# Optimization experiments

Measured on AMD Instinct MI355X. Metric: run time of the kernel, lower is better.

Reference implementation:

```python
import jax, jax.numpy as jnp
import numpy as np

EMBED_DIM = 2048
NUM_HEADS = 16
HEAD_DIM = EMBED_DIM // NUM_HEADS


def setup_inputs() -> dict:
    key = jax.random.key(0)
    k_x, k_qkv, k_out = jax.random.split(key, 3)
    x = jax.random.normal(k_x, (4, 2048, EMBED_DIM), dtype=jnp.float32)
    # torch nn.Linear(in, out) weight is [out, in]; y = x @ W.T
    scale = 1.0 / np.sqrt(EMBED_DIM)
    W_qkv = jax.random.uniform(k_qkv, (3 * EMBED_DIM, EMBED_DIM), dtype=jnp.float32, minval=-scale, maxval=scale)
    W_out = jax.random.uniform(k_out, (EMBED_DIM, EMBED_DIM), dtype=jnp.float32, minval=-scale, maxval=scale)
    return {"x": x, "W_qkv": W_qkv, "W_out": W_out}


def reference(x, W_qkv, W_out):
    B, T, C = x.shape
    H, D = NUM_HEADS, HEAD_DIM
    qkv = jnp.einsum("btc,fc->btf", x, W_qkv)  # [B,T,3C]
    q, k, v = jnp.split(qkv, 3, axis=-1)
    q = q.reshape(B, T, H, D).transpose(0, 2, 1, 3)  # [B,H,T,D]
    k = k.reshape(B, T, H, D).transpose(0, 2, 1, 3)
    v = v.reshape(B, T, H, D).transpose(0, 2, 1, 3)
    att = jnp.einsum("bhqd,bhkd->bhqk", q, k) / jnp.sqrt(jnp.float32(D))
    causal = jnp.tril(jnp.ones((T, T), dtype=bool))
    att = jnp.where(causal[None, None], att, -jnp.inf)
    att = jax.nn.softmax(att, axis=-1)
    out = jnp.einsum("bhqk,bhkd->bhqd", att, v)  # [B,H,T,D]
    out = out.transpose(0, 2, 1, 3).reshape(B, T, C)
    return jnp.einsum("btc,oc->bto", out, W_out)
```

## Files before the change

### kernel.cpp

```cpp
#include <hip/hip_runtime.h>
#include <hip/hip_bf16.h>
#include <math.h>

#define BDIM 4
#define TDIM 2048
#define CDIM 2048
#define HDIM 16
#define DDIM 128
#define MROWS (BDIM*TDIM)
#define NQKV (3*CDIM)
#define GK   CDIM
#define QSZ  (MROWS*CDIM)

#define NTILES 32
#define NITER  16
#define HT     8192
#define BOFF   32768

#define QSCALE 0.1275171f

typedef __attribute__((ext_vector_type(8))) short short8;
typedef __attribute__((ext_vector_type(4))) unsigned short ushort4v;
typedef __attribute__((ext_vector_type(4))) float f32x4;

__device__ __forceinline__ unsigned short f2bf(float f) {
    unsigned int u = __float_as_uint(f);
    u += 0x7fffu + ((u >> 16) & 1u);
    return (unsigned short)(u >> 16);
}

__device__ __forceinline__ void gload16(const unsigned short* g, unsigned short* l) {
    __builtin_amdgcn_global_load_lds((__attribute__((address_space(1))) void*)(g),
                                     (__attribute__((address_space(3))) void*)(l),
                                     16, 0, 0);
}

__global__ __launch_bounds__(256) void cvt_bf16(const float* __restrict__ in,
                                                unsigned short* __restrict__ outp,
                                                int n4, int sbound)
{
    const int stride = gridDim.x * blockDim.x;
    for (int i = blockIdx.x * blockDim.x + threadIdx.x; i < n4; i += stride) {
        float4 f = ((const float4*)in)[i];
        const float s = (i < sbound) ? QSCALE : 1.0f;
        ushort4v u;
        u[0] = f2bf(f.x*s); u[1] = f2bf(f.y*s); u[2] = f2bf(f.z*s); u[3] = f2bf(f.w*s);
        ((ushort4v*)outp)[i] = u;
    }
}

__device__ __forceinline__ void stage_half(const unsigned short* __restrict__ T,
                                           int rowbase, int kcol,
                                           unsigned short* dst, int w, int lane)
{
    const int sw = ((lane & 3) ^ ((lane >> 3) & 3)) * 8;
#pragma unroll
    for (int j = 0; j < 2; ++j) {
        const int r = w*32 + j*16 + (lane >> 2);
        gload16(T + (size_t)(rowbase + r)*GK + kcol + sw, dst + (w*32 + j*16)*32);
    }
}

template<int MQ, int KS, int BUF, bool RDB, bool WAIT>
__device__ __forceinline__ void gphase(unsigned short* lds,
    const unsigned short* __restrict__ stT, int stRow, int stKcol, unsigned short* stDst,
    int wr, int wc, int fr, int colu, int w, int lane,
    short8 (&bfr)[4], f32x4 (&acc)[8][4])
{
    const unsigned short* Ah = lds + (BUF*2 + KS)*HT;
    const unsigned short* Bh = lds + BOFF + (BUF*2 + KS)*HT;
    short8 af[4];
#pragma unroll
    for (int mi = 0; mi < 4; ++mi)
        af[mi] = *(const short8*)&Ah[(wr*128 + (MQ*4 + mi)*16 + fr)*32 + colu];
    if (RDB) {
#pragma unroll
        for (int nj = 0; nj < 4; ++nj)
            bfr[nj] = *(const short8*)&Bh[(wc*64 + nj*16 + fr)*32 + colu];
    }
    stage_half(stT, stRow, stKcol, stDst, w, lane);
    if (WAIT) asm volatile("s_waitcnt vmcnt(4)" ::: "memory");
    __builtin_amdgcn_s_barrier();
    asm volatile("s_waitcnt lgkmcnt(0)" ::: "memory");
    __builtin_amdgcn_sched_barrier(0);
    __builtin_amdgcn_s_setprio(1);
#pragma unroll
    for (int mi = 0; mi < 4; ++mi)
#pragma unroll
        for (int nj = 0; nj < 4; ++nj)
            acc[MQ*4 + mi][nj] = __builtin_amdgcn_mfma_f32_16x16x32_bf16(af[mi], bfr[nj], acc[MQ*4 + mi][nj], 0, 0, 0);
    __builtin_amdgcn_s_setprio(0);
    __builtin_amdgcn_s_barrier();
}

template<int MODE>
__global__ __launch_bounds__(512, 2) void gemm8(const unsigned short* __restrict__ A,
                                                const unsigned short* __restrict__ B,
                                                float* __restrict__ outp,
                                                unsigned short* __restrict__ qb,
                                                unsigned short* __restrict__ kb,
                                                unsigned short* __restrict__ vt,
                                                int Nsz)
{
    extern __shared__ unsigned short lds[];
    const int tid  = threadIdx.x;
    const int w    = tid >> 6;
    const int lane = tid & 63;
    const int wr   = w >> 2, wc = w & 3;
    const int fr   = lane & 15;
    const int fg   = lane >> 4;
    const int colu = (fg ^ ((fr >> 1) & 3)) * 8;
    const int m0   = blockIdx.x * 256, n0 = blockIdx.y * 256;

    f32x4 acc[8][4];
#pragma unroll
    for (int i = 0; i < 8; ++i)
#pragma unroll
        for (int j = 0; j < 4; ++j) acc[i][j] = (f32x4)(0.f);
    short8 bfr[4];

    stage_half(A, m0, 0,  lds,             w, lane);
    stage_half(B, n0, 0,  lds + BOFF,      w, lane);
    stage_half(A, m0, 32, lds + HT,        w, lane);
    stage_half(B, n0, 32, lds + BOFF + HT, w, lane);
    stage_half(A, m0, 64, lds + 2*HT,        w, lane);
    stage_half(B, n0, 64, lds + BOFF + 2*HT, w, lane);
    asm volatile("s_waitcnt vmcnt(0)" ::: "memory");
    __builtin_amdgcn_s_barrier();

    for (int i = 0; i < NITER; ++i) {
        const int t1 = 2*i + 1;
        const int t2 = (2*i + 2 < NTILES) ? 2*i + 2 : 0;
        const int t3 = (2*i + 3 < NTILES) ? 2*i + 3 : 0;
        gphase<0,0,0,true ,false>(lds, A, m0, t1*64+32, lds + 3*HT,        wr, wc, fr, colu, w, lane, bfr, acc);
        gphase<1,0,0,false,false>(lds, B, n0, t1*64+32, lds + BOFF + 3*HT, wr, wc, fr, colu, w, lane, bfr, acc);
        gphase<0,1,0,true ,false>(lds, A, m0, t2*64,    lds,               wr, wc, fr, colu, w, lane, bfr, acc);
        gphase<1,1,0,false,true >(lds, B, n0, t2*64,    lds + BOFF,        wr, wc, fr, colu, w, lane, bfr, acc);
        gphase<0,0,1,true ,false>(lds, A, m0, t2*64+32, lds + HT,          wr, wc, fr, colu, w, lane, bfr, acc);
        gphase<1,0,1,false,false>(lds, B, n0, t2*64+32, lds + BOFF + HT,   wr, wc, fr, colu, w, lane, bfr, acc);
        gphase<0,1,1,true ,false>(lds, A, m0, t3*64,    lds + 2*HT,        wr, wc, fr, colu, w, lane, bfr, acc);
        gphase<1,1,1,false,true >(lds, B, n0, t3*64,    lds + BOFF + 2*HT, wr, wc, fr, colu, w, lane, bfr, acc);
    }
    asm volatile("s_waitcnt vmcnt(0)" ::: "memory");

    if (MODE == 0) {
#pragma unroll
        for (int mi = 0; mi < 8; ++mi)
#pragma unroll
            for (int nj = 0; nj < 4; ++nj) {
                const int n   = n0 + wc*64 + nj*16 + fr;
                const int sel = n >> 11;
                const int c   = n & 2047;
                const int hh  = c >> 7, dd = c & 127;
                const int mb  = m0 + wr*128 + mi*16 + fg*4;
                const int bb  = mb >> 11, tt = mb & 2047;
                if (sel == 2) {
                    ushort4v v;
#pragma unroll
                    for (int r = 0; r < 4; ++r) v[r] = f2bf(acc[mi][nj][r]);
                    *(ushort4v*)&vt[((size_t)(bb*HDIM + hh)*DDIM + dd)*TDIM + tt] = v;
                } else {
                    unsigned short* dstb = (sel == 0) ? qb : kb;
#pragma unroll
                    for (int r = 0; r < 4; ++r)
                        dstb[((size_t)(bb*HDIM + hh)*TDIM + tt + r)*DDIM + dd] = f2bf(acc[mi][nj][r]);
                }
            }
    } else {
#pragma unroll
        for (int mi = 0; mi < 8; ++mi)
#pragma unroll
            for (int nj = 0; nj < 4; ++nj) {
                const int n = n0 + wc*64 + nj*16 + fr;
#pragma unroll
                for (int r = 0; r < 4; ++r) {
                    const int m = m0 + wr*128 + mi*16 + fg*4 + r;
                    outp[(size_t)m*Nsz + n] = acc[mi][nj][r];
                }
            }
    }
}

__global__ __launch_bounds__(512) void attn_mfma(const unsigned short* __restrict__ Qg,
                                                 const unsigned short* __restrict__ Kg,
                                                 const unsigned short* __restrict__ Vt,
                                                 unsigned short* __restrict__ attb)
{
    extern __shared__ unsigned short smem[];
    unsigned short* KsB = smem;
    unsigned short* Vs  = smem + 16384;
    unsigned short* Ps  = smem + 24576;

    const int tid  = threadIdx.x;
    const int w    = tid >> 6;
    const int lane = tid & 63;
    const int g    = lane >> 4;
    const int c    = lane & 15;
    const int bh   = blockIdx.x & 63;
    const int qb_  = 15 - (blockIdx.x >> 6);
    const int q0   = qb_ * 128;
    const int qt   = 2*qb_ + 1;
    const int qw   = q0 + w*16;

    const unsigned short* Kbh  = Kg + (size_t)bh*TDIM*DDIM;
    const unsigned short* Vtbh = Vt + (size_t)bh*DDIM*TDIM;

    short8 qf[4];
    {
        const unsigned short* qrow = Qg + ((size_t)bh*TDIM + qw + c)*DDIM + g*8;
#pragma unroll
        for (int s = 0; s < 4; ++s)
            qf[s] = *(const short8*)(qrow + s*32);
    }

    f32x4 oacc[8];
#pragma unroll
    for (int i = 0; i < 8; ++i) oacc[i] = (f32x4)(0.f);
    float m_r[4], l_r[4];
#pragma unroll
    for (int r = 0; r < 4; ++r) { m_r[r] = -INFINITY; l_r[r] = 0.f; }

#define STAGE_K(buf, kt_)                                                        \
    {                                                                            \
        _Pragma("unroll")                                                        \
        for (int j = 0; j < 2; ++j) {                                            \
            const int rw  = (w<<3) + (j<<2) + (lane >> 4);                       \
            const int sub = (lane & 15) ^ (rw & 7);                              \
            gload16(Kbh + ((size_t)((kt_)*64 + rw))*DDIM + sub*8,                \
                    &KsB[(buf)*8192 + ((w<<3) + (j<<2))*128]);                   \
        }                                                                        \
    }
#define STAGE_V(kt_)                                                             \
    {                                                                            \
        _Pragma("unroll")                                                        \
        for (int j = 0; j < 2; ++j) {                                            \
            const int d   = (w<<4) + (j<<3) + (lane >> 3);                       \
            const int sub = (lane & 7) ^ (d & 7);                                \
            gload16(Vtbh + (size_t)d*TDIM + (kt_)*64 + sub*8,                    \
                    &Vs[((w<<4) + (j<<3))*64]);                                  \
        }                                                                        \
    }

    STAGE_K(0, 0);
    STAGE_V(0);
    __syncthreads();

    for (int kt = 0; kt <= qt; ++kt) {
        const int cur = kt & 1;
        if (kt < qt) STAGE_K(cur ^ 1, kt + 1);
        if (kt > 0)  STAGE_V(kt);

        const bool active = (kt*64) <= (qw + 15);
        short8 pf[2];

        if (active) {
            f32x4 sa[4];
#pragma unroll
            for (int n = 0; n < 4; ++n) sa[n] = (f32x4)(0.f);
#pragma unroll
            for (int s = 0; s < 4; ++s)
#pragma unroll
                for (int n = 0; n < 4; ++n) {
                    const int row = n*16 + c;
                    short8 bf = *(const short8*)&KsB[cur*8192 + ((row*128 + s*32 + g*8) ^ ((row&7)<<3))];
                    sa[n] = __builtin_amdgcn_mfma_f32_16x16x32_bf16(qf[s], bf, sa[n], 0, 0, 0);
                }

            if (kt*64 + 63 > qw) {
#pragma unroll
                for (int n = 0; n < 4; ++n) {
                    const int kgl = kt*64 + n*16 + c;
#pragma unroll
                    for (int r = 0; r < 4; ++r) {
                        const int qgl = qw + g*4 + r;
                        if (kgl > qgl) sa[n][r] = -INFINITY;
                    }
                }
            }

            float corr[4];
#pragma unroll
            for (int r = 0; r < 4; ++r) {
                float mx = fmaxf(fmaxf(sa[0][r], sa[1][r]), fmaxf(sa[2][r], sa[3][r]));
                mx = fmaxf(mx, __shfl_xor(mx, 1));
                mx = fmaxf(mx, __shfl_xor(mx, 2));
                mx = fmaxf(mx, __shfl_xor(mx, 4));
                mx = fmaxf(mx, __shfl_xor(mx, 8));
                const float mn = fmaxf(m_r[r], mx);
                corr[r] = exp2f(m_r[r] - mn);
                float rs = 0.f;
#pragma unroll
                for (int n = 0; n < 4; ++n) {
                    const float p = exp2f(sa[n][r] - mn);
                    sa[n][r] = p;
                    rs += p;
                }
                rs += __shfl_xor(rs, 1);
                rs += __shfl_xor(rs, 2);
                rs += __shfl_xor(rs, 4);
                rs += __shfl_xor(rs, 8);
                l_r[r] = l_r[r]*corr[r] + rs;
                m_r[r] = mn;
            }
#pragma unroll
            for (int i = 0; i < 8; ++i) {
                f32x4 o = oacc[i];
                o[0] *= corr[0]; o[1] *= corr[1]; o[2] *= corr[2]; o[3] *= corr[3];
                oacc[i] = o;
            }

            unsigned short* Pw = &Ps[w*1024];
#pragma unroll
            for (int n = 0; n < 4; ++n)
#pragma unroll
                for (int r = 0; r < 4; ++r) {
                    const int q = g*4 + r, k = n*16 + c;
                    Pw[(q*64 + k) ^ ((q&7)<<3)] = f2bf(sa[n][r]);
                }
#pragma unroll
            for (int s2 = 0; s2 < 2; ++s2)
                pf[s2] = *(const short8*)&Pw[(c*64 + s2*32 + g*8) ^ ((c&7)<<3)];
        }

        __syncthreads();

        if (active) {
#pragma unroll
            for (int s2 = 0; s2 < 2; ++s2)
#pragma unroll
                for (int dt = 0; dt < 8; ++dt) {
                    const int d = dt*16 + c;
                    short8 vf = *(const short8*)&Vs[(d*64 + s2*32 + g*8) ^ ((d&7)<<3)];
                    oacc[dt] = __builtin_amdgcn_mfma_f32_16x16x32_bf16(pf[s2], vf, oacc[dt], 0, 0, 0);
                }
        }

        __syncthreads();
    }

    float inv[4];
#pragma unroll
    for (int r = 0; r < 4; ++r) inv[r] = 1.f / l_r[r];
    const int b = bh >> 4, h = bh & 15;
    unsigned short* obase = attb + ((size_t)b*TDIM + qw + g*4)*CDIM + h*DDIM + c;
#pragma unroll
    for (int dt = 0; dt < 8; ++dt)
#pragma unroll
        for (int r = 0; r < 4; ++r)
            obase[(size_t)r*CDIM + dt*16] = f2bf(oacc[dt][r] * inv[r]);
}

extern "C" void kernel_launch(void* const* d_in, const int* in_sizes, int n_in,
                              void* d_out, int out_size, void* d_ws, size_t ws_size,
                              hipStream_t stream)
{
    const float* x    = (const float*)d_in[0];
    const float* Wqkv = (const float*)d_in[1];
    const float* Wout = (const float*)d_in[2];
    float* out = (float*)d_out;

    unsigned short* ws = (unsigned short*)d_ws;
    unsigned short* xb    = ws;
    unsigned short* Wqkvb = xb    + (size_t)MROWS*CDIM;
    unsigned short* Woutb = Wqkvb + (size_t)NQKV*CDIM;
    unsigned short* Qb    = Woutb + (size_t)CDIM*CDIM;
    unsigned short* Kb    = Qb + QSZ;
    unsigned short* Vtb   = Kb + QSZ;
    unsigned short* attb  = Vtb + QSZ;

    cvt_bf16<<<2048, 256, 0, stream>>>(x,    xb,    MROWS*CDIM/4, 0);
    cvt_bf16<<<2048, 256, 0, stream>>>(Wqkv, Wqkvb, NQKV*CDIM/4, CDIM*CDIM/4);
    cvt_bf16<<<1024, 256, 0, stream>>>(Wout, Woutb, CDIM*CDIM/4, 0);
    gemm8<0><<<dim3(MROWS/256, NQKV/256), 512, 131072, stream>>>(xb, Wqkvb, nullptr, Qb, Kb, Vtb, NQKV);
    attn_mfma<<<dim3(64*16), 512, 65536, stream>>>(Qb, Kb, Vtb, attb);
    gemm8<1><<<dim3(MROWS/256, CDIM/256), 512, 131072, stream>>>(attb, Woutb, out, nullptr, nullptr, nullptr, CDIM);
}
```

Before: 458.8 us.

## Double-buffer V tiles, lazily rescale softmax, and compute row sums via MFMA

V tiles are now double-buffered like K, which removes one of the two block barriers per key tile and lets V loads for the next tile overlap compute. The online softmax skips the max reduction and accumulator rescale unless some probability exceeds a threshold (the lazy-rescale trick). Row sums are computed by an MFMA against a vector of ones instead of shuffle reductions. Shared memory rises from 64 KB to 80 KB per block, which may lower occupancy. The lazy rescale keeps results exact but lets intermediate values grow larger before renormalising.

```diff
diff --git a/kernel.cpp b/kernel.cpp
--- a/kernel.cpp
+++ b/kernel.cpp
@@ -188,8 +188,8 @@
 {
     extern __shared__ unsigned short smem[];
     unsigned short* KsB = smem;
-    unsigned short* Vs  = smem + 16384;
-    unsigned short* Ps  = smem + 24576;
+    unsigned short* VsB = smem + 16384;
+    unsigned short* Ps  = smem + 32768;
 
     const int tid  = threadIdx.x;
     const int w    = tid >> 6;
@@ -213,6 +213,10 @@
             qf[s] = *(const short8*)(qrow + s*32);
     }
 
+    short8 onesf;
+#pragma unroll
+    for (int j = 0; j < 8; ++j) onesf[j] = (short)0x3F80;
+
     f32x4 oacc[8];
 #pragma unroll
     for (int i = 0; i < 8; ++i) oacc[i] = (f32x4)(0.f);
@@ -230,28 +234,26 @@
                     &KsB[(buf)*8192 + ((w<<3) + (j<<2))*128]);                   \
         }                                                                        \
     }
-#define STAGE_V(kt_)                                                             \
+#define STAGE_V(buf, kt_)                                                        \
     {                                                                            \
         _Pragma("unroll")                                                        \
         for (int j = 0; j < 2; ++j) {                                            \
             const int d   = (w<<4) + (j<<3) + (lane >> 3);                       \
             const int sub = (lane & 7) ^ (d & 7);                                \
             gload16(Vtbh + (size_t)d*TDIM + (kt_)*64 + sub*8,                    \
-                    &Vs[((w<<4) + (j<<3))*64]);                                  \
+                    &VsB[(buf)*8192 + ((w<<4) + (j<<3))*64]);                    \
         }                                                                        \
     }
 
     STAGE_K(0, 0);
-    STAGE_V(0);
+    STAGE_V(0, 0);
     __syncthreads();
 
     for (int kt = 0; kt <= qt; ++kt) {
         const int cur = kt & 1;
-        if (kt < qt) STAGE_K(cur ^ 1, kt + 1);
-        if (kt > 0)  STAGE_V(kt);
+        if (kt < qt) { STAGE_K(cur ^ 1, kt + 1); STAGE_V(cur ^ 1, kt + 1); }
 
         const bool active = (kt*64) <= (qw + 15);
-        short8 pf[2];
 
         if (active) {
             f32x4 sa[4];
@@ -278,35 +280,48 @@
                 }
             }
 
-            float corr[4];
-#pragma unroll
-            for (int r = 0; r < 4; ++r) {
-                float mx = fmaxf(fmaxf(sa[0][r], sa[1][r]), fmaxf(sa[2][r], sa[3][r]));
-                mx = fmaxf(mx, __shfl_xor(mx, 1));
-                mx = fmaxf(mx, __shfl_xor(mx, 2));
-                mx = fmaxf(mx, __shfl_xor(mx, 4));
-                mx = fmaxf(mx, __shfl_xor(mx, 8));
-                const float mn = fmaxf(m_r[r], mx);
-                corr[r] = exp2f(m_r[r] - mn);
-                float rs = 0.f;
-#pragma unroll
-                for (int n = 0; n < 4; ++n) {
-                    const float p = exp2f(sa[n][r] - mn);
-                    sa[n][r] = p;
-                    rs += p;
-                }
-                rs += __shfl_xor(rs, 1);
-                rs += __shfl_xor(rs, 2);
-                rs += __shfl_xor(rs, 4);
-                rs += __shfl_xor(rs, 8);
-                l_r[r] = l_r[r]*corr[r] + rs;
-                m_r[r] = mn;
-            }
-#pragma unroll
-            for (int i = 0; i < 8; ++i) {
-                f32x4 o = oacc[i];
-                o[0] *= corr[0]; o[1] *= corr[1]; o[2] *= corr[2]; o[3] *= corr[3];
-                oacc[i] = o;
+            f32x4 p[4];
+            bool slow = (kt == 0);
+            if (!slow) {
+#pragma unroll
+                for (int n = 0; n < 4; ++n)
+#pragma unroll
+                    for (int r = 0; r < 4; ++r)
+                        p[n][r] = exp2f(sa[n][r] - m_r[r]);
+                float pm = p[0][0];
+#pragma unroll
+                for (int n = 0; n < 4; ++n)
+#pragma unroll
+                    for (int r = 0; r < 4; ++r)
+                        pm = fmaxf(pm, p[n][r]);
+                slow = __any(pm > 256.0f);
+            }
+            if (slow) {
+                float corr[4];
+#pragma unroll
+                for (int r = 0; r < 4; ++r) {
+                    float mx = fmaxf(fmaxf(sa[0][r], sa[1][r]), fmaxf(sa[2][r], sa[3][r]));
+                    mx = fmaxf(mx, __shfl_xor(mx, 1));
+                    mx = fmaxf(mx, __shfl_xor(mx, 2));
+                    mx = fmaxf(mx, __shfl_xor(mx, 4));
+                    mx = fmaxf(mx, __shfl_xor(mx, 8));
+                    const float mn = fmaxf(m_r[r], mx);
+                    corr[r] = exp2f(m_r[r] - mn);
+                    m_r[r] = mn;
+                }
+#pragma unroll
+                for (int n = 0; n < 4; ++n)
+#pragma unroll
+                    for (int r = 0; r < 4; ++r)
+                        p[n][r] = exp2f(sa[n][r] - m_r[r]);
+#pragma unroll
+                for (int i = 0; i < 8; ++i) {
+                    f32x4 o = oacc[i];
+                    o[0] *= corr[0]; o[1] *= corr[1]; o[2] *= corr[2]; o[3] *= corr[3];
+                    oacc[i] = o;
+                }
+#pragma unroll
+                for (int r = 0; r < 4; ++r) l_r[r] *= corr[r];
             }
 
             unsigned short* Pw = &Ps[w*1024];
@@ -315,22 +330,25 @@
 #pragma unroll
                 for (int r = 0; r < 4; ++r) {
                     const int q = g*4 + r, k = n*16 + c;
-                    Pw[(q*64 + k) ^ ((q&7)<<3)] = f2bf(sa[n][r]);
-                }
+                    Pw[(q*64 + k) ^ ((q&7)<<3)] = f2bf(p[n][r]);
+                }
+            short8 pf[2];
 #pragma unroll
             for (int s2 = 0; s2 < 2; ++s2)
                 pf[s2] = *(const short8*)&Pw[(c*64 + s2*32 + g*8) ^ ((c&7)<<3)];
-        }
-
-        __syncthreads();
-
-        if (active) {
+
+            f32x4 rs = (f32x4)(0.f);
+            rs = __builtin_amdgcn_mfma_f32_16x16x32_bf16(pf[0], onesf, rs, 0, 0, 0);
+            rs = __builtin_amdgcn_mfma_f32_16x16x32_bf16(pf[1], onesf, rs, 0, 0, 0);
+#pragma unroll
+            for (int r = 0; r < 4; ++r) l_r[r] += rs[r];
+
 #pragma unroll
             for (int s2 = 0; s2 < 2; ++s2)
 #pragma unroll
                 for (int dt = 0; dt < 8; ++dt) {
                     const int d = dt*16 + c;
-                    short8 vf = *(const short8*)&Vs[(d*64 + s2*32 + g*8) ^ ((d&7)<<3)];
+                    short8 vf = *(const short8*)&VsB[cur*8192 + ((d*64 + s2*32 + g*8) ^ ((d&7)<<3))];
                     oacc[dt] = __builtin_amdgcn_mfma_f32_16x16x32_bf16(pf[s2], vf, oacc[dt], 0, 0, 0);
                 }
         }
@@ -372,6 +390,6 @@
     cvt_bf16<<<2048, 256, 0, stream>>>(Wqkv, Wqkvb, NQKV*CDIM/4, CDIM*CDIM/4);
     cvt_bf16<<<1024, 256, 0, stream>>>(Wout, Woutb, CDIM*CDIM/4, 0);
     gemm8<0><<<dim3(MROWS/256, NQKV/256), 512, 131072, stream>>>(xb, Wqkvb, nullptr, Qb, Kb, Vtb, NQKV);
-    attn_mfma<<<dim3(64*16), 512, 65536, stream>>>(Qb, Kb, Vtb, attb);
+    attn_mfma<<<dim3(64*16), 512, 81920, stream>>>(Qb, Kb, Vtb, attb);
     gemm8<1><<<dim3(MROWS/256, CDIM/256), 512, 131072, stream>>>(attb, Woutb, out, nullptr, nullptr, nullptr, CDIM);
 }
```

Result: faster. 417.0 us (-9.1%).
